# Kernel tuning notes

Measured on AMD Instinct MI355X. Metric: run time of the kernel, lower is better.

## Reference

```python
import jax, jax.numpy as jnp
import numpy as np

ALPHA = 0.2  # leaky-relu negative slope
N_NODES = 50000
IN_F = 256
OUT_F = 64
N_EDGES = 1600000


def setup_inputs() -> dict:
    key = jax.random.key(0)
    k1, k2, k3, k4 = jax.random.split(key, 4)
    x = jax.random.normal(k1, (N_NODES, IN_F), dtype=jnp.float32)
    # xavier_normal-ish scales for params
    W = jax.random.normal(k2, (IN_F, OUT_F), dtype=jnp.float32) * (1.414 * (2.0 / (IN_F + OUT_F)) ** 0.5)
    a = jax.random.normal(k3, (1, 2 * OUT_F), dtype=jnp.float32) * (1.414 * (2.0 / (1 + 2 * OUT_F)) ** 0.5)
    edge_index = jax.random.randint(k4, (2, N_EDGES), 0, N_NODES, dtype=jnp.int64)
    return {"x": x, "W": W, "a": a, "edge_index": edge_index}


def reference(x, W, a, edge_index):
    N = x.shape[0]
    src = edge_index[0]  # row index of sparse adjacency (aggregation target)
    dst = edge_index[1]  # column index (neighbor being gathered)
    h = x @ W  # [N, out]
    out_f = h.shape[1]
    # a @ cat(h[src], h[dst]) == (h @ a1)[src] + (h @ a2)[dst]
    a1 = a[0, :out_f]
    a2 = a[0, out_f:]
    s_src = h @ a1  # [N]
    s_dst = h @ a2  # [N]
    score = s_src[src] + s_dst[dst]  # [E]
    edge_e = jnp.exp(-jax.nn.leaky_relu(score, negative_slope=ALPHA))  # [E]
    # e_rowsum[i] = sum_{e: src==i} edge_e[e]
    e_rowsum = jax.ops.segment_sum(edge_e, src, num_segments=N)  # [N]
    # h_prime[i] = sum_{e: src==i} edge_e[e] * h[dst[e]]
    h_prime = jax.ops.segment_sum(edge_e[:, None] * h[dst], src, num_segments=N)  # [N, out]
    h_prime = h_prime / e_rowsum[:, None]
    return jax.nn.elu(h_prime)
```

## Files before the change

kernel.cpp:

```cpp
#include <hip/hip_runtime.h>
#include <hip/hip_bf16.h>
#include <hip/hip_fp16.h>


#define ALPHA 0.2f
#define KDIM 256
#define FDIM 64
#define BIN_CHUNK 8192
#define BUCKET_CAP 4096

typedef __bf16 bf16x8 __attribute__((ext_vector_type(8)));
typedef float f32x4 __attribute__((ext_vector_type(4)));
typedef unsigned int u32;
typedef unsigned short u16;

__global__ __launch_bounds__(256) void gat_wt_kernel(
    const float* __restrict__ W, __hip_bfloat16* __restrict__ w_t)
{
    const int t = blockIdx.x * 256 + threadIdx.x;
    if (t < KDIM * FDIM) {
        const int k = t >> 6;
        const int n = t & 63;
        w_t[n * KDIM + k] = __float2bfloat16(W[t]);
    }
}

__global__ __launch_bounds__(256) void gat_gemm_kernel(
    const float* __restrict__ x, const __hip_bfloat16* __restrict__ w_tp,
    const float* __restrict__ a, __hip_bfloat16* __restrict__ h_bf,
    float* __restrict__ s_src, float* __restrict__ s_dst, int N)
{
    const int lane = threadIdx.x & 63;
    const int wv = threadIdx.x >> 6;
    const int m0 = blockIdx.x * 64 + wv * 16;
    const int c = lane & 15;
    const int q = lane >> 4;

    const int mrow = m0 + c;
    const float* xp = x + (long)(mrow < N ? mrow : N - 1) * KDIM;
    const __bf16* wt = (const __bf16*)w_tp;

    f32x4 acc[4];
#pragma unroll
    for (int ct = 0; ct < 4; ++ct) acc[ct] = (f32x4){0.f, 0.f, 0.f, 0.f};

#pragma unroll 2
    for (int kc = 0; kc < 8; ++kc) {
        const int k0 = kc * 32 + q * 8;
        const float4 xa = *(const float4*)(xp + k0);
        const float4 xb = *(const float4*)(xp + k0 + 4);
        bf16x8 af;
        af[0] = (__bf16)xa.x; af[1] = (__bf16)xa.y;
        af[2] = (__bf16)xa.z; af[3] = (__bf16)xa.w;
        af[4] = (__bf16)xb.x; af[5] = (__bf16)xb.y;
        af[6] = (__bf16)xb.z; af[7] = (__bf16)xb.w;
#pragma unroll
        for (int ct = 0; ct < 4; ++ct) {
            const bf16x8 bf = *(const bf16x8*)(wt + (ct * 16 + c) * KDIM + k0);
            acc[ct] = __builtin_amdgcn_mfma_f32_16x16x32_bf16(af, bf, acc[ct], 0, 0, 0);
        }
    }

    float a1c[4], a2c[4];
#pragma unroll
    for (int ct = 0; ct < 4; ++ct) {
        a1c[ct] = a[ct * 16 + c];
        a2c[ct] = a[FDIM + ct * 16 + c];
    }
    float s1r[4], s2r[4];
#pragma unroll
    for (int reg = 0; reg < 4; ++reg) {
        float s1 = 0.f, s2 = 0.f;
#pragma unroll
        for (int ct = 0; ct < 4; ++ct) {
            s1 += acc[ct][reg] * a1c[ct];
            s2 += acc[ct][reg] * a2c[ct];
        }
        s1r[reg] = s1; s2r[reg] = s2;
    }
#pragma unroll
    for (int off = 1; off < 16; off <<= 1) {
#pragma unroll
        for (int reg = 0; reg < 4; ++reg) {
            s1r[reg] += __shfl_xor(s1r[reg], off);
            s2r[reg] += __shfl_xor(s2r[reg], off);
        }
    }

#pragma unroll
    for (int reg = 0; reg < 4; ++reg) {
        const int row = m0 + q * 4 + reg;
        if (row < N) {
#pragma unroll
            for (int ct = 0; ct < 4; ++ct)
                h_bf[(long)row * FDIM + ct * 16 + c] = __float2bfloat16(acc[ct][reg]);
            if (c == 0) { s_src[row] = s1r[reg]; s_dst[row] = s2r[reg]; }
        }
    }
}

__global__ __launch_bounds__(256) void gat_bhist_kernel(
    const int* __restrict__ srcA, int* __restrict__ bcnt, int E, int NBU)
{
    __shared__ int hist[1024];
    const int t = threadIdx.x;
    for (int j = t; j < 1024; j += 256) hist[j] = 0;
    __syncthreads();
    const int base = blockIdx.x * BIN_CHUNK;
    const int cnt = min(BIN_CHUNK, E - base);
    for (int i = t; i < cnt; i += 256)
        atomicAdd(&hist[srcA[base + i] >> 6], 1);
    __syncthreads();
    for (int j = t; j < NBU; j += 256) {
        const int v = hist[j];
        if (v) atomicAdd(&bcnt[j], v);
    }
}

__global__ __launch_bounds__(256) void gat_bscan_kernel(
    const int* __restrict__ bcnt, int* __restrict__ bbase, int* __restrict__ bcur)
{
    __shared__ int wsum[4];
    const int t = threadIdx.x;
    const int lane = t & 63;
    const int w = t >> 6;
    const int4 v = *(const int4*)&bcnt[4 * t];
    const int tsum = v.x + v.y + v.z + v.w;
    int incl = tsum;
#pragma unroll
    for (int off = 1; off < 64; off <<= 1) {
        const int nv = __shfl_up(incl, off);
        if (lane >= off) incl += nv;
    }
    if (lane == 63) wsum[w] = incl;
    __syncthreads();
    int woff = 0;
    if (w > 0) woff += wsum[0];
    if (w > 1) woff += wsum[1];
    if (w > 2) woff += wsum[2];
    const int e0 = woff + incl - tsum;
    const int4 o = make_int4(e0, e0 + v.x, e0 + v.x + v.y, e0 + v.x + v.y + v.z);
    *(int4*)&bbase[4 * t] = o;
    *(int4*)&bcur[4 * t] = o;
    if (t == 255) bbase[1024] = e0 + tsum;
}

__global__ __launch_bounds__(256) void gat_bin_kernel(
    const int* __restrict__ srcA, const int* __restrict__ dstA,
    int* __restrict__ bcur, u32* __restrict__ pair, int E, int NBU)
{
    __shared__ int hist[1024];
    __shared__ int lcur[1024];
    const int t = threadIdx.x;
    for (int j = t; j < 1024; j += 256) hist[j] = 0;
    __syncthreads();
    const int base = blockIdx.x * BIN_CHUNK;
    const int cnt = min(BIN_CHUNK, E - base);
    for (int i = t; i < cnt; i += 256)
        atomicAdd(&hist[srcA[base + i] >> 6], 1);
    __syncthreads();
    for (int j = t; j < NBU; j += 256) {
        const int v = hist[j];
        lcur[j] = v ? atomicAdd(&bcur[j], v) : 0;
    }
    __syncthreads();
    for (int i = t; i < cnt; i += 256) {
        const int s = srcA[base + i];
        const int d = dstA[base + i];
        const int pos = atomicAdd(&lcur[s >> 6], 1);
        pair[pos] = ((u32)(s & 63) << 16) | (u32)d;
    }
}

__global__ __launch_bounds__(256) void gat_bsort_kernel(
    const u32* __restrict__ pair, const int* __restrict__ bbase,
    const float* __restrict__ s_src, const float* __restrict__ s_dst,
    int* __restrict__ offs, u32* __restrict__ sorted_pk, int N, int NBU)
{
    __shared__ u32 chunk[BUCKET_CAP];
    __shared__ int cur[64];
    __shared__ float ssl[64];

    const int b = blockIdx.x;
    const int t = threadIdx.x;
    const int s0 = b << 6;
    const int e0 = bbase[b];
    const int e1 = bbase[b + 1];
    const int n = min(e1 - e0, BUCKET_CAP);

    if (t < 64) {
        cur[t] = 0;
        ssl[t] = (s0 + t < N) ? s_src[s0 + t] : 0.f;
    }
    __syncthreads();
    for (int i = t; i < n; i += 256) {
        const u32 p = pair[e0 + i];
        chunk[i] = p;
        atomicAdd(&cur[p >> 16], 1);
    }
    __syncthreads();
    if (t < 64) {
        const int v = cur[t];
        int incl = v;
#pragma unroll
        for (int off = 1; off < 64; off <<= 1) {
            const int nv = __shfl_up(incl, off);
            if (t >= off) incl += nv;
        }
        const int excl = incl - v;
        if (s0 + t < N) offs[s0 + t] = e0 + excl;
        cur[t] = excl;
    }
    if (b == NBU - 1 && t == 0) offs[N] = e1;
    __syncthreads();
    for (int i = t; i < n; i += 256) {
        const u32 p = chunk[i];
        const int sl = p >> 16;
        const int d = (int)(p & 0xFFFFu);
        const int slot = atomicAdd(&cur[sl], 1);
        const float sc = ssl[sl] + s_dst[d];
        const float lr = sc > 0.f ? sc : ALPHA * sc;
        const float wgt = __expf(-lr);
        const u32 wh = (u32)__half_as_ushort(__float2half(wgt));
        sorted_pk[e0 + slot] = (u32)d | (wh << 16);
    }
}

__global__ __launch_bounds__(256) void gat_gather_kernel(
    const int* __restrict__ offs, const u32* __restrict__ sorted_pk,
    const __hip_bfloat16* __restrict__ h_bf, float* __restrict__ out, int N)
{
    const int node = blockIdx.x * 4 + (threadIdx.x >> 6);
    if (node >= N) return;
    const int lane = threadIdx.x & 63;
    const int q = lane >> 3;
    const int c = lane & 7;

    const int start = offs[node];
    const int end = offs[node + 1];
    const __bf16* hb = (const __bf16*)h_bf;

    float acc[8];
#pragma unroll
    for (int j = 0; j < 8; ++j) acc[j] = 0.f;
    float wsum = 0.f;

#pragma unroll 2
    for (int e = start + q; e < end; e += 8) {
        const u32 p = sorted_pk[e];
        const float wgt = __half2float(__ushort_as_half((u16)(p >> 16)));
        const int d = (int)(p & 0xFFFFu);
        const bf16x8 hv = *(const bf16x8*)(hb + (long)d * FDIM + 8 * c);
#pragma unroll
        for (int j = 0; j < 8; ++j) acc[j] += wgt * (float)hv[j];
        wsum += wgt;
    }

#pragma unroll
    for (int off = 8; off < 64; off <<= 1) {
#pragma unroll
        for (int j = 0; j < 8; ++j) acc[j] += __shfl_xor(acc[j], off);
        wsum += __shfl_xor(wsum, off);
    }

    if (q == 0) {
        const float inv = 1.0f / wsum;
        float o[8];
#pragma unroll
        for (int j = 0; j < 8; ++j) {
            const float v = acc[j] * inv;
            o[j] = v > 0.f ? v : expm1f(v);
        }
        float* op = &out[(long)node * FDIM + 8 * c];
        *(float4*)op = make_float4(o[0], o[1], o[2], o[3]);
        *(float4*)(op + 4) = make_float4(o[4], o[5], o[6], o[7]);
    }
}

extern "C" void kernel_launch(void* const* d_in, const int* in_sizes, int n_in,
                              void* d_out, int out_size, void* d_ws, size_t ws_size,
                              hipStream_t stream) {
    const float* x = (const float*)d_in[0];
    const float* W = (const float*)d_in[1];
    const float* a = (const float*)d_in[2];
    const int* ei  = (const int*)d_in[3];

    const int N = in_sizes[0] / KDIM;
    const int E = in_sizes[3] / 2;
    const int NBU = (N + 63) >> 6;
    const int NBLK = (E + BIN_CHUNK - 1) / BIN_CHUNK;
    const int* srcA = ei;
    const int* dstA = ei + E;

    __hip_bfloat16* h_bf = (__hip_bfloat16*)d_ws;
    __hip_bfloat16* w_t  = h_bf + (size_t)N * FDIM;
    float* s_src = (float*)(w_t + KDIM * FDIM);
    float* s_dst = s_src + N;
    int* offs    = (int*)(s_dst + N);
    int* bcnt    = offs + N + 4;
    int* bbase   = bcnt + 1024;
    int* bcur    = bbase + 1028;
    u32* pair    = (u32*)(bcur + 1024);
    u32* sorted_pk = pair + E;
    float* out   = (float*)d_out;

    hipMemsetAsync(bcnt, 0, 1024 * sizeof(int), stream);

    gat_wt_kernel<<<dim3((KDIM * FDIM + 255) / 256), dim3(256), 0, stream>>>(W, w_t);
    gat_gemm_kernel<<<dim3((N + 63) / 64), dim3(256), 0, stream>>>(
        x, w_t, a, h_bf, s_src, s_dst, N);

    gat_bhist_kernel<<<dim3(NBLK), dim3(256), 0, stream>>>(srcA, bcnt, E, NBU);
    gat_bscan_kernel<<<dim3(1), dim3(256), 0, stream>>>(bcnt, bbase, bcur);
    gat_bin_kernel<<<dim3(NBLK), dim3(256), 0, stream>>>(srcA, dstA, bcur, pair, E, NBU);
    gat_bsort_kernel<<<dim3(NBU), dim3(256), 0, stream>>>(
        pair, bbase, s_src, s_dst, offs, sorted_pk, N, NBU);

    gat_gather_kernel<<<dim3((N + 3) / 4), dim3(256), 0, stream>>>(
        offs, sorted_pk, h_bf, out, N);
}
```

Baseline: 210.8 us.

## Fuse bucket sort with gather and stage bin inputs in shared memory

The per-bucket sort kernel now also does the weighted neighbor aggregation. Sorted edges stay in LDS instead of being written to a global sorted array and read back through an offsets array. The binning kernel caches packed src/dst pairs in shared memory so it reads the edge list once instead of twice, and the bin chunk size is doubled. The cost is fewer blocks in the gather phase: one block of 4 waves handles 64 nodes, 16 per wave serially. LDS use also rises, which may reduce occupancy and the parallelism available to hide latency on the h gathers.

```diff
diff --git a/kernel.cpp b/kernel.cpp
--- a/kernel.cpp
+++ b/kernel.cpp
@@ -6,7 +6,7 @@
 #define ALPHA 0.2f
 #define KDIM 256
 #define FDIM 64
-#define BIN_CHUNK 8192
+#define BIN_CHUNK 16384
 #define BUCKET_CAP 4096
 
 typedef __bf16 bf16x8 __attribute__((ext_vector_type(8)));
@@ -149,6 +149,7 @@
     const int* __restrict__ srcA, const int* __restrict__ dstA,
     int* __restrict__ bcur, u32* __restrict__ pair, int E, int NBU)
 {
+    __shared__ u32 chunk[BIN_CHUNK];
     __shared__ int hist[1024];
     __shared__ int lcur[1024];
     const int t = threadIdx.x;
@@ -156,8 +157,12 @@
     __syncthreads();
     const int base = blockIdx.x * BIN_CHUNK;
     const int cnt = min(BIN_CHUNK, E - base);
-    for (int i = t; i < cnt; i += 256)
-        atomicAdd(&hist[srcA[base + i] >> 6], 1);
+    for (int i = t; i < cnt; i += 256) {
+        const int s = srcA[base + i];
+        const int d = dstA[base + i];
+        chunk[i] = ((u32)(s >> 6) << 22) | ((u32)(s & 63) << 16) | (u32)d;
+        atomicAdd(&hist[s >> 6], 1);
+    }
     __syncthreads();
     for (int j = t; j < NBU; j += 256) {
         const int v = hist[j];
@@ -165,20 +170,21 @@
     }
     __syncthreads();
     for (int i = t; i < cnt; i += 256) {
-        const int s = srcA[base + i];
-        const int d = dstA[base + i];
-        const int pos = atomicAdd(&lcur[s >> 6], 1);
-        pair[pos] = ((u32)(s & 63) << 16) | (u32)d;
-    }
-}
-
-__global__ __launch_bounds__(256) void gat_bsort_kernel(
+        const u32 p = chunk[i];
+        const int pos = atomicAdd(&lcur[p >> 22], 1);
+        pair[pos] = p & 0x003FFFFFu;
+    }
+}
+
+__global__ __launch_bounds__(256) void gat_bgather_kernel(
     const u32* __restrict__ pair, const int* __restrict__ bbase,
     const float* __restrict__ s_src, const float* __restrict__ s_dst,
-    int* __restrict__ offs, u32* __restrict__ sorted_pk, int N, int NBU)
-{
-    __shared__ u32 chunk[BUCKET_CAP];
+    const __hip_bfloat16* __restrict__ h_bf, float* __restrict__ out, int N)
+{
+    __shared__ u32 raw[BUCKET_CAP];
+    __shared__ u32 spk[BUCKET_CAP];
     __shared__ int cur[64];
+    __shared__ int seg[65];
     __shared__ float ssl[64];
 
     const int b = blockIdx.x;
@@ -195,7 +201,7 @@
     __syncthreads();
     for (int i = t; i < n; i += 256) {
         const u32 p = pair[e0 + i];
-        chunk[i] = p;
+        raw[i] = p;
         atomicAdd(&cur[p >> 16], 1);
     }
     __syncthreads();
@@ -208,13 +214,13 @@
             if (t >= off) incl += nv;
         }
         const int excl = incl - v;
-        if (s0 + t < N) offs[s0 + t] = e0 + excl;
+        seg[t] = excl;
         cur[t] = excl;
-    }
-    if (b == NBU - 1 && t == 0) offs[N] = e1;
+        if (t == 63) seg[64] = incl;
+    }
     __syncthreads();
     for (int i = t; i < n; i += 256) {
-        const u32 p = chunk[i];
+        const u32 p = raw[i];
         const int sl = p >> 16;
         const int d = (int)(p & 0xFFFFu);
         const int slot = atomicAdd(&cur[sl], 1);
@@ -222,58 +228,58 @@
         const float lr = sc > 0.f ? sc : ALPHA * sc;
         const float wgt = __expf(-lr);
         const u32 wh = (u32)__half_as_ushort(__float2half(wgt));
-        sorted_pk[e0 + slot] = (u32)d | (wh << 16);
-    }
-}
-
-__global__ __launch_bounds__(256) void gat_gather_kernel(
-    const int* __restrict__ offs, const u32* __restrict__ sorted_pk,
-    const __hip_bfloat16* __restrict__ h_bf, float* __restrict__ out, int N)
-{
-    const int node = blockIdx.x * 4 + (threadIdx.x >> 6);
-    if (node >= N) return;
-    const int lane = threadIdx.x & 63;
+        spk[slot] = (u32)d | (wh << 16);
+    }
+    __syncthreads();
+
+    const int w = t >> 6;
+    const int lane = t & 63;
     const int q = lane >> 3;
     const int c = lane & 7;
-
-    const int start = offs[node];
-    const int end = offs[node + 1];
     const __bf16* hb = (const __bf16*)h_bf;
 
-    float acc[8];
-#pragma unroll
-    for (int j = 0; j < 8; ++j) acc[j] = 0.f;
-    float wsum = 0.f;
+    for (int ln = 0; ln < 16; ++ln) {
+        const int nl = w * 16 + ln;
+        const int node = s0 + nl;
+        if (node >= N) break;
+        const int start = seg[nl];
+        const int end = seg[nl + 1];
+
+        float acc[8];
+#pragma unroll
+        for (int j = 0; j < 8; ++j) acc[j] = 0.f;
+        float wsum = 0.f;
 
 #pragma unroll 2
-    for (int e = start + q; e < end; e += 8) {
-        const u32 p = sorted_pk[e];
-        const float wgt = __half2float(__ushort_as_half((u16)(p >> 16)));
-        const int d = (int)(p & 0xFFFFu);
-        const bf16x8 hv = *(const bf16x8*)(hb + (long)d * FDIM + 8 * c);
-#pragma unroll
-        for (int j = 0; j < 8; ++j) acc[j] += wgt * (float)hv[j];
-        wsum += wgt;
-    }
-
-#pragma unroll
-    for (int off = 8; off < 64; off <<= 1) {
-#pragma unroll
-        for (int j = 0; j < 8; ++j) acc[j] += __shfl_xor(acc[j], off);
-        wsum += __shfl_xor(wsum, off);
-    }
-
-    if (q == 0) {
-        const float inv = 1.0f / wsum;
-        float o[8];
-#pragma unroll
-        for (int j = 0; j < 8; ++j) {
-            const float v = acc[j] * inv;
-            o[j] = v > 0.f ? v : expm1f(v);
-        }
-        float* op = &out[(long)node * FDIM + 8 * c];
-        *(float4*)op = make_float4(o[0], o[1], o[2], o[3]);
-        *(float4*)(op + 4) = make_float4(o[4], o[5], o[6], o[7]);
+        for (int e = start + q; e < end; e += 8) {
+            const u32 p = spk[e];
+            const float wgt = __half2float(__ushort_as_half((u16)(p >> 16)));
+            const int d = (int)(p & 0xFFFFu);
+            const bf16x8 hv = *(const bf16x8*)(hb + (long)d * FDIM + 8 * c);
+#pragma unroll
+            for (int j = 0; j < 8; ++j) acc[j] += wgt * (float)hv[j];
+            wsum += wgt;
+        }
+
+#pragma unroll
+        for (int off = 8; off < 64; off <<= 1) {
+#pragma unroll
+            for (int j = 0; j < 8; ++j) acc[j] += __shfl_xor(acc[j], off);
+            wsum += __shfl_xor(wsum, off);
+        }
+
+        if (q == 0) {
+            const float inv = 1.0f / wsum;
+            float o[8];
+#pragma unroll
+            for (int j = 0; j < 8; ++j) {
+                const float v = acc[j] * inv;
+                o[j] = v > 0.f ? v : expm1f(v);
+            }
+            float* op = &out[(long)node * FDIM + 8 * c];
+            *(float4*)op = make_float4(o[0], o[1], o[2], o[3]);
+            *(float4*)(op + 4) = make_float4(o[4], o[5], o[6], o[7]);
+        }
     }
 }
 
@@ -296,12 +302,10 @@
     __hip_bfloat16* w_t  = h_bf + (size_t)N * FDIM;
     float* s_src = (float*)(w_t + KDIM * FDIM);
     float* s_dst = s_src + N;
-    int* offs    = (int*)(s_dst + N);
-    int* bcnt    = offs + N + 4;
+    int* bcnt    = (int*)(s_dst + N);
     int* bbase   = bcnt + 1024;
     int* bcur    = bbase + 1028;
     u32* pair    = (u32*)(bcur + 1024);
-    u32* sorted_pk = pair + E;
     float* out   = (float*)d_out;
 
     hipMemsetAsync(bcnt, 0, 1024 * sizeof(int), stream);
@@ -313,9 +317,6 @@
     gat_bhist_kernel<<<dim3(NBLK), dim3(256), 0, stream>>>(srcA, bcnt, E, NBU);
     gat_bscan_kernel<<<dim3(1), dim3(256), 0, stream>>>(bcnt, bbase, bcur);
     gat_bin_kernel<<<dim3(NBLK), dim3(256), 0, stream>>>(srcA, dstA, bcur, pair, E, NBU);
-    gat_bsort_kernel<<<dim3(NBU), dim3(256), 0, stream>>>(
-        pair, bbase, s_src, s_dst, offs, sorted_pk, N, NBU);
-
-    gat_gather_kernel<<<dim3((N + 3) / 4), dim3(256), 0, stream>>>(
-        offs, sorted_pk, h_bf, out, N);
-}
+    gat_bgather_kernel<<<dim3(NBU), dim3(256), 0, stream>>>(
+        pair, bbase, s_src, s_dst, h_bf, out, N);
+}
```

Result: slower. 219.6 us (+4.2%).
